# Performance work log

Hardware: AMD Instinct MI355X
Metric: run time of the kernel (lower is better)

## Reference

```python
import math
import jax, jax.numpy as jnp
import numpy as np

B, N, D, H, NUM_N, NUM_J = 16, 1024, 128, 8, 8, 4
PRE_S = 2.0


def setup_inputs() -> dict:
    key = jax.random.key(0)
    ks = jax.random.split(key, 12)
    g = lambda i, shape: jax.random.normal(ks[i], shape, jnp.float32) * 0.02
    return {
        "eigenvector": jax.random.normal(ks[0], (B, N, N), jnp.float32),
        "eigenvalue": jax.random.uniform(ks[1], (B, N), jnp.float32, minval=0.0, maxval=2.0),
        "length": jax.random.randint(ks[2], (B,), N // 2, N).at[0].set(N),
        "eig_w_W": g(3, (D, D + 1)), "eig_w_b": jnp.zeros((D,), jnp.float32),
        "ln1_s": jnp.ones((D,), jnp.float32), "ln1_b": jnp.zeros((D,), jnp.float32),
        "ln2_s": jnp.ones((D,), jnp.float32), "ln2_b": jnp.zeros((D,), jnp.float32),
        "qkv_W": g(4, (3 * D, D)), "qkv_b": jnp.zeros((3 * D,), jnp.float32),
        "out_W": g(5, (D, D)), "out_b": jnp.zeros((D,), jnp.float32),
        "ffn_W1": g(6, (D, D)), "ffn_b1": jnp.zeros((D,), jnp.float32),
        "ffn_W2": g(7, (D, D)), "ffn_b2": jnp.zeros((D,), jnp.float32),
        "dec_sca_W": g(8, (NUM_N, D)), "dec_sca_b": jnp.zeros((NUM_N,), jnp.float32),
        "dec_wav_W": g(9, (NUM_N, D)), "dec_wav_b": jnp.zeros((NUM_N,), jnp.float32),
        "dec_scl_W": g(10, (NUM_J, D)), "dec_scl_b": jnp.zeros((NUM_J,), jnp.float32),
    }


def _layernorm(x, s, b):
    m = x.mean(-1, keepdims=True)
    v = ((x - m) ** 2).mean(-1, keepdims=True)
    return (x - m) / jnp.sqrt(v + 1e-5) * s + b


def _gen_base(y, num_n):
    # Chebyshev-style recurrence; returns (base_wavelet, base_scaling), each [B, num_n, ...y.shape[1:]]
    t_even = jnp.ones_like(y)
    t_odd = y
    wav, sca = [t_even], [t_odd]
    for _ in range(num_n - 1):
        t_even = 2.0 * y * t_odd - t_even
        t_odd = 2.0 * y * t_even - t_odd
        wav.append(t_even)
        sca.append(t_odd)
    return jnp.stack(wav, 1), jnp.stack(sca, 1)


def _forward(eigenvalue, length,
             eig_w_W, eig_w_b, ln1_s, ln1_b, ln2_s, ln2_b,
             qkv_W, qkv_b, out_W, out_b, ffn_W1, ffn_b1, ffn_W2, ffn_b2,
             dec_sca_W, dec_sca_b, dec_wav_W, dec_wav_b, dec_scl_W, dec_scl_b):
    eva = eigenvalue  # [B, N], max(length) == N by construction
    pad = jnp.arange(N)[None, :] >= length[:, None]  # [B, N], True = padded key

    # --- SineEncoding ---
    div = jnp.exp(jnp.arange(0, D, 2).astype(jnp.float32) * (-math.log(10000.0) / D))  # [D/2]
    pe = (eva * 100.0)[:, :, None] * div  # [B, N, D/2]
    eeig = jnp.concatenate([eva[:, :, None], jnp.sin(pe), jnp.cos(pe)], -1)  # [B, N, D+1]
    eig = eeig @ eig_w_W.T + eig_w_b  # [B, N, D]

    # --- MHA block (pre-norm, key padding mask) ---
    h = _layernorm(eig, ln1_s, ln1_b)
    q, k, v = jnp.split(h @ qkv_W.T + qkv_b, 3, axis=-1)
    dh = D // H
    rh = lambda t: t.reshape(B, N, H, dh)
    scores = jnp.einsum('bqhd,bkhd->bhqk', rh(q), rh(k)) / math.sqrt(dh)
    scores = jnp.where(pad[:, None, None, :], -1e9, scores)  # finite mask (padded rows zeroed later)
    attn = jax.nn.softmax(scores, axis=-1)
    mo = jnp.einsum('bhqk,bkhd->bqhd', attn, rh(v)).reshape(B, N, D) @ out_W.T + out_b
    eig = eig + mo

    # --- FFN block ---
    f = _layernorm(eig, ln2_s, ln2_b)
    f = jax.nn.gelu(f @ ffn_W1.T + ffn_b1, approximate=False) @ ffn_W2.T + ffn_b2
    eig = eig + f

    lenf = length.astype(jnp.float32)[:, None]

    def pooled(W, b):
        c = eig @ W.T + b
        c = jnp.where(pad[:, :, None], 0.0, c)
        return c.sum(1) / (lenf + 1e-8)

    coe_sca = jax.nn.sigmoid(pooled(dec_sca_W, dec_sca_b))  # [B, NUM_N]
    coe_sca = coe_sca / (coe_sca.sum(-1, keepdims=True) + 1e-8)
    coe_wav = jax.nn.sigmoid(pooled(dec_wav_W, dec_wav_b))
    coe_wav = coe_wav / (coe_wav.sum(-1, keepdims=True) + 1e-8)
    coe_scl = jax.nn.sigmoid(pooled(dec_scl_W, dec_scl_b)) * PRE_S  # [B, NUM_J]

    _, base_scaling = _gen_base(eva[:, :, None] - 1.0, NUM_N)  # [B, NUM_N, N, 1]
    fsw = eva[:, :, None] * coe_scl[:, None, :]  # [B, N, NUM_J]
    fsw = jnp.where(fsw > 2.0, 0.0, fsw)
    base_wavelet, _ = _gen_base(fsw - 1.0, NUM_N)  # [B, NUM_N, N, NUM_J]

    base_scaling = 0.5 * (1.0 - base_scaling)
    base_wavelet = 0.5 * (1.0 - base_wavelet)
    curr_s = jnp.einsum('bn,bnxj->bxj', coe_sca, base_scaling)  # [B, N, 1]
    curr_w = jnp.einsum('bn,bnxj->bxj', coe_wav, base_wavelet)  # [B, N, NUM_J]
    out = jnp.concatenate([curr_s, curr_w], -1)  # [B, N, 1+NUM_J]
    out = out / (jnp.linalg.norm(out, axis=-1, keepdims=True) + 1e-8)  # tight_frames
    return out


def reference(eigenvector, eigenvalue, length,
              eig_w_W, eig_w_b, ln1_s, ln1_b, ln2_s, ln2_b,
              qkv_W, qkv_b, out_W, out_b, ffn_W1, ffn_b1, ffn_W2, ffn_b2,
              dec_sca_W, dec_sca_b, dec_wav_W, dec_wav_b, dec_scl_W, dec_scl_b):
    # eigenvector (evc_dense) is passed through unchanged in the original; the learned
    # output is filter_signals_after, which we return.
    return _forward(eigenvalue, length,
                    eig_w_W, eig_w_b, ln1_s, ln1_b, ln2_s, ln2_b,
                    qkv_W, qkv_b, out_W, out_b, ffn_W1, ffn_b1, ffn_W2, ffn_b2,
                    dec_sca_W, dec_sca_b, dec_wav_W, dec_wav_b, dec_scl_W, dec_scl_b)
```

## Files before the change

kernel.cpp:

```cpp
#include <hip/hip_runtime.h>
#include <math.h>

#define NB 16
#define NN 1024
#define ND 128
#define NH 8
#define DH 16

typedef float f32x4 __attribute__((ext_vector_type(4)));
typedef short s16x4 __attribute__((ext_vector_type(4)));

static __device__ __forceinline__ ushort f2bf(float x) {
  unsigned u = __float_as_uint(x);
  u = (u + 0x7FFFu + ((u >> 16) & 1u)) >> 16;
  return (ushort)u;
}

static __device__ __forceinline__ float exp2h(float x) {
  return __builtin_amdgcn_exp2f(x);
}

static __device__ __forceinline__ f32x4 mfma16(s16x4 a, s16x4 b, f32x4 c) {
  return __builtin_amdgcn_mfma_f32_16x16x16bf16_1k(a, b, c, 0, 0, 0);
}

static __device__ __forceinline__ s16x4 pack_bf4(float p0, float p1, float p2,
                                                 float p3) {
  s16x4 r = {(short)f2bf(p0), (short)f2bf(p1), (short)f2bf(p2),
             (short)f2bf(p3)};
  return r;
}

#define QSCALE 0.36067376022224085f

__global__ __launch_bounds__(256) void kW(
    const float* __restrict__ eW, const float* __restrict__ qkvW,
    const float* __restrict__ outW, const float* __restrict__ W1,
    const float* __restrict__ W2, ushort* __restrict__ wbf) {
  int i = blockIdx.x * 256 + threadIdx.x;
  if (i < 18432) {
    int r = i / 144, k = i - r * 144;
    wbf[i] = (k < 129) ? f2bf(eW[r * 129 + k]) : (ushort)0;
  } else if (i < 67584) {
    wbf[i] = f2bf(qkvW[i - 18432]);
  } else if (i < 83968) {
    wbf[i] = f2bf(outW[i - 67584]);
  } else if (i < 100352) {
    wbf[i] = f2bf(W1[i - 83968]);
  } else if (i < 116736) {
    wbf[i] = f2bf(W2[i - 100352]);
  }
}

__global__ __launch_bounds__(256, 4) void kA(
    const float* __restrict__ eva, const ushort* __restrict__ eWbf,
    const float* __restrict__ eb, const float* __restrict__ g1s,
    const float* __restrict__ g1b, const ushort* __restrict__ qkvbf,
    const float* __restrict__ qb, float* __restrict__ eig,
    ushort* __restrict__ qg, ushort* __restrict__ kg,
    ushort* __restrict__ vt) {
  __shared__ __align__(16) ushort ee[32][148];
  __shared__ __align__(16) float eig_f[32][132];
  __shared__ __align__(16) ushort hbf[32][132];
  int t = threadIdx.x;
  int rows0 = blockIdx.x * 32;
  int w = t >> 6, l = t & 63, g = l >> 4, c = l & 15;

  {
    int d = t & 63, r0 = t >> 6;
    float div = __expf((float)(2 * d) * (-9.210340371976184f / 128.0f));
#pragma unroll
    for (int k = 0; k < 8; ++k) {
      int row = r0 + 4 * k;
      float e = eva[rows0 + row];
      float pe = e * 100.0f * div;
      ee[row][1 + d] = f2bf(__sinf(pe));
      ee[row][65 + d] = f2bf(__cosf(pe));
      if (d == 0) ee[row][0] = f2bf(e);
    }
  }
  for (int i = t; i < 32 * 19; i += 256) {
    int row = i / 19, cc = 129 + (i - row * 19);
    ee[row][cc] = 0;
  }
  __syncthreads();

  {
    int rt = w >> 1;
#pragma unroll
    for (int i = 0; i < 4; ++i) {
      int ct = (w & 1) * 4 + i;
      f32x4 st = {0.f, 0.f, 0.f, 0.f};
#pragma unroll
      for (int kk = 0; kk < 9; ++kk) {
        s16x4 xf = *(const s16x4*)&ee[rt * 16 + c][kk * 16 + g * 4];
        s16x4 yf = *(const s16x4*)&eWbf[(ct * 16 + c) * 144 + kk * 16 + g * 4];
        st = mfma16(xf, yf, st);
      }
      float bias = eb[ct * 16 + c];
#pragma unroll
      for (int j = 0; j < 4; ++j)
        eig_f[rt * 16 + g * 4 + j][ct * 16 + c] = st[j] + bias;
    }
  }
  __syncthreads();

#pragma unroll
  for (int p = 0; p < 4; ++p) {
    int idx = p * 256 + t;
    int row = idx >> 5, c4 = idx & 31;
    *(float4*)&eig[(size_t)(rows0 + row) * ND + c4 * 4] =
        *(const float4*)&eig_f[row][c4 * 4];
  }

  {
    int row = t >> 3, s = t & 7;
    float vals[16];
    float sum = 0.f;
#pragma unroll
    for (int k = 0; k < 16; ++k) {
      vals[k] = eig_f[row][s + 8 * k];
      sum += vals[k];
    }
    sum += __shfl_xor(sum, 1, 8);
    sum += __shfl_xor(sum, 2, 8);
    sum += __shfl_xor(sum, 4, 8);
    float mean = sum * (1.0f / 128.0f);
    float sq = 0.f;
#pragma unroll
    for (int k = 0; k < 16; ++k) {
      float d = vals[k] - mean;
      sq += d * d;
    }
    sq += __shfl_xor(sq, 1, 8);
    sq += __shfl_xor(sq, 2, 8);
    sq += __shfl_xor(sq, 4, 8);
    float rstd = rsqrtf(sq * (1.0f / 128.0f) + 1e-5f);
#pragma unroll
    for (int k = 0; k < 16; ++k) {
      int col = s + 8 * k;
      hbf[row][col] = f2bf((vals[k] - mean) * rstd * g1s[col] + g1b[col]);
    }
  }
  __syncthreads();

  {
    int rt = w >> 1;
    int b = rows0 >> 10, nn0 = rows0 & 1023;
#pragma unroll
    for (int i = 0; i < 12; ++i) {
      int ct = (w & 1) * 12 + i;
      f32x4 st = {0.f, 0.f, 0.f, 0.f};
#pragma unroll
      for (int kk = 0; kk < 8; ++kk) {
        s16x4 xf = *(const s16x4*)&hbf[rt * 16 + c][kk * 16 + g * 4];
        s16x4 yf = *(const s16x4*)&qkvbf[(ct * 16 + c) * 128 + kk * 16 + g * 4];
        st = mfma16(xf, yf, st);
      }
      float bias = qb[ct * 16 + c];
      int which = ct >> 3, head = ct & 7;
      if (which == 2) {
        unsigned lo = (unsigned)f2bf(st[0] + bias) |
                      ((unsigned)f2bf(st[1] + bias) << 16);
        unsigned hi = (unsigned)f2bf(st[2] + bias) |
                      ((unsigned)f2bf(st[3] + bias) << 16);
        uint2 pk;
        pk.x = lo;
        pk.y = hi;
        *(uint2*)(vt + ((size_t)(b * NH + head) * DH + c) * NN + nn0 +
                  rt * 16 + g * 4) = pk;
      } else {
        ushort* dst = which == 0 ? qg : kg;
        float sc = which == 0 ? QSCALE : 1.0f;
        size_t base =
            ((size_t)(b * NH + head) * NN + nn0 + rt * 16 + g * 4) * DH + c;
#pragma unroll
        for (int j = 0; j < 4; ++j)
          dst[base + j * DH] = f2bf((st[j] + bias) * sc);
      }
    }
  }
}

__global__ __launch_bounds__(512) void k_attn(
    const ushort* __restrict__ qg, const ushort* __restrict__ kg,
    const ushort* __restrict__ vt, const int* __restrict__ length,
    ushort* __restrict__ att) {
  __shared__ ushort Ksh[128][20];
  __shared__ ushort VTsh[16][136];
  int bid = blockIdx.x;
  int bh = bid >> 3, qc = bid & 7;
  int b = bh >> 3, h = bh & 7;
  int t = threadIdx.x;
  int w = t >> 6, l = t & 63, g = l >> 4, c = l & 15;
  int len = length[b];
  int qrow = qc * 128 + w * 16 + c;
  s16x4 qf = *(const s16x4*)(qg + ((size_t)bh * NN + qrow) * DH + g * 4);
  f32x4 oacc = {0.f, 0.f, 0.f, 0.f};
  float lsum = 0.f;
  int ksr = t >> 2, ksc = t & 3;
  int vr = t >> 5, vc = t & 31;
  const ushort* kbg = kg + (size_t)bh * NN * DH;
  const ushort* vbg = vt + (size_t)bh * DH * NN;
  for (int t0 = 0; t0 < len; t0 += 128) {
    *(uint2*)&Ksh[ksr][ksc * 4] =
        *(const uint2*)(kbg + (size_t)(t0 + ksr) * DH + ksc * 4);
    *(uint2*)&VTsh[vr][vc * 4] =
        *(const uint2*)(vbg + (size_t)vr * NN + t0 + vc * 4);
    __syncthreads();
    if (t0 + 128 <= len) {
#pragma unroll
      for (int kt = 0; kt < 8; ++kt) {
        s16x4 kf = *(const s16x4*)&Ksh[kt * 16 + c][g * 4];
        f32x4 st = {0.f, 0.f, 0.f, 0.f};
        st = mfma16(kf, qf, st);
        float p0 = exp2h(st[0]), p1 = exp2h(st[1]);
        float p2 = exp2h(st[2]), p3 = exp2h(st[3]);
        lsum += (p0 + p1) + (p2 + p3);
        s16x4 pf = pack_bf4(p0, p1, p2, p3);
        s16x4 vf = *(const s16x4*)&VTsh[c][kt * 16 + g * 4];
        oacc = mfma16(vf, pf, oacc);
      }
    } else {
      for (int kt = 0; kt < 8 && t0 + kt * 16 < len; ++kt) {
        s16x4 kf = *(const s16x4*)&Ksh[kt * 16 + c][g * 4];
        f32x4 st = {0.f, 0.f, 0.f, 0.f};
        st = mfma16(kf, qf, st);
        int kj = t0 + kt * 16 + g * 4;
        float p0 = (kj + 0 < len) ? exp2h(st[0]) : 0.f;
        float p1 = (kj + 1 < len) ? exp2h(st[1]) : 0.f;
        float p2 = (kj + 2 < len) ? exp2h(st[2]) : 0.f;
        float p3 = (kj + 3 < len) ? exp2h(st[3]) : 0.f;
        lsum += (p0 + p1) + (p2 + p3);
        s16x4 pf = pack_bf4(p0, p1, p2, p3);
        s16x4 vf = *(const s16x4*)&VTsh[c][kt * 16 + g * 4];
        oacc = mfma16(vf, pf, oacc);
      }
    }
    __syncthreads();
  }
  lsum += __shfl_xor(lsum, 16, 64);
  lsum += __shfl_xor(lsum, 32, 64);
  float inv = 1.0f / lsum;
  s16x4 ob = pack_bf4(oacc[0] * inv, oacc[1] * inv, oacc[2] * inv,
                      oacc[3] * inv);
  *(s16x4*)(att + ((size_t)b * NN + qrow) * ND + h * DH + g * 4) = ob;
}

__global__ __launch_bounds__(256, 4) void kB(
    const ushort* __restrict__ attg, const ushort* __restrict__ outbf,
    const float* __restrict__ ob, const float* __restrict__ g2s,
    const float* __restrict__ g2b, const ushort* __restrict__ w1bf,
    const float* __restrict__ fb1, const ushort* __restrict__ w2bf,
    const float* __restrict__ fb2, const float* __restrict__ eig,
    const int* __restrict__ length, float* __restrict__ bsum) {
  __shared__ __align__(16) ushort attb[32][136];
  __shared__ __align__(16) float eig_f[32][132];
  __shared__ __align__(16) ushort hbf[32][132];
  __shared__ float csum[2][128];
  int t = threadIdx.x;
  int rows0 = blockIdx.x * 32;
  int w = t >> 6, l = t & 63, g = l >> 4, c = l & 15;
  int rt = w >> 1;

#pragma unroll
  for (int p = 0; p < 2; ++p) {
    int idx = p * 256 + t;
    int row = idx >> 4, c8 = idx & 15;
    *(uint4*)&attb[row][c8 * 8] =
        *(const uint4*)&attg[(size_t)(rows0 + row) * ND + c8 * 8];
  }
#pragma unroll
  for (int p = 0; p < 4; ++p) {
    int idx = p * 256 + t;
    int row = idx >> 5, c4 = idx & 31;
    *(float4*)&eig_f[row][c4 * 4] =
        *(const float4*)&eig[(size_t)(rows0 + row) * ND + c4 * 4];
  }
  __syncthreads();

#pragma unroll
  for (int i = 0; i < 4; ++i) {
    int ct = (w & 1) * 4 + i;
    f32x4 st = {0.f, 0.f, 0.f, 0.f};
#pragma unroll
    for (int kk = 0; kk < 8; ++kk) {
      s16x4 xf = *(const s16x4*)&attb[rt * 16 + c][kk * 16 + g * 4];
      s16x4 yf = *(const s16x4*)&outbf[(ct * 16 + c) * 128 + kk * 16 + g * 4];
      st = mfma16(xf, yf, st);
    }
    float bias = ob[ct * 16 + c];
#pragma unroll
    for (int j = 0; j < 4; ++j) {
      int row = rt * 16 + g * 4 + j, col = ct * 16 + c;
      eig_f[row][col] = st[j] + bias + eig_f[row][col];
    }
  }
  __syncthreads();

  {
    int row = t >> 3, s = t & 7;
    float vals[16];
    float sum = 0.f;
#pragma unroll
    for (int k = 0; k < 16; ++k) {
      vals[k] = eig_f[row][s + 8 * k];
      sum += vals[k];
    }
    sum += __shfl_xor(sum, 1, 8);
    sum += __shfl_xor(sum, 2, 8);
    sum += __shfl_xor(sum, 4, 8);
    float mean = sum * (1.0f / 128.0f);
    float sq = 0.f;
#pragma unroll
    for (int k = 0; k < 16; ++k) {
      float d = vals[k] - mean;
      sq += d * d;
    }
    sq += __shfl_xor(sq, 1, 8);
    sq += __shfl_xor(sq, 2, 8);
    sq += __shfl_xor(sq, 4, 8);
    float rstd = rsqrtf(sq * (1.0f / 128.0f) + 1e-5f);
#pragma unroll
    for (int k = 0; k < 16; ++k) {
      int col = s + 8 * k;
      hbf[row][col] = f2bf((vals[k] - mean) * rstd * g2s[col] + g2b[col]);
    }
  }
  __syncthreads();

#pragma unroll
  for (int i = 0; i < 4; ++i) {
    int ct = (w & 1) * 4 + i;
    f32x4 st = {0.f, 0.f, 0.f, 0.f};
#pragma unroll
    for (int kk = 0; kk < 8; ++kk) {
      s16x4 xf = *(const s16x4*)&hbf[rt * 16 + c][kk * 16 + g * 4];
      s16x4 yf = *(const s16x4*)&w1bf[(ct * 16 + c) * 128 + kk * 16 + g * 4];
      st = mfma16(xf, yf, st);
    }
    float bias = fb1[ct * 16 + c];
#pragma unroll
    for (int j = 0; j < 4; ++j) {
      float gv = st[j] + bias;
      attb[rt * 16 + g * 4 + j][ct * 16 + c] =
          f2bf(0.5f * gv * (1.0f + erff(gv * 0.7071067811865475f)));
    }
  }
  __syncthreads();

#pragma unroll
  for (int i = 0; i < 4; ++i) {
    int ct = (w & 1) * 4 + i;
    f32x4 st = {0.f, 0.f, 0.f, 0.f};
#pragma unroll
    for (int kk = 0; kk < 8; ++kk) {
      s16x4 xf = *(const s16x4*)&attb[rt * 16 + c][kk * 16 + g * 4];
      s16x4 yf = *(const s16x4*)&w2bf[(ct * 16 + c) * 128 + kk * 16 + g * 4];
      st = mfma16(xf, yf, st);
    }
    float bias = fb2[ct * 16 + c];
#pragma unroll
    for (int j = 0; j < 4; ++j) {
      int row = rt * 16 + g * 4 + j, col = ct * 16 + c;
      eig_f[row][col] = st[j] + bias + eig_f[row][col];
    }
  }
  __syncthreads();

  {
    int b = rows0 >> 10, n0 = rows0 & 1023;
    int len = length[b];
    int col = t & 127, half = t >> 7;
    float s = 0.f;
#pragma unroll
    for (int r = 0; r < 16; ++r) {
      int row = half * 16 + r;
      if (n0 + row < len) s += eig_f[row][col];
    }
    csum[half][col] = s;
  }
  __syncthreads();
  if (t < 128) bsum[(size_t)blockIdx.x * 128 + t] = csum[0][t] + csum[1][t];
}

__global__ __launch_bounds__(128) void kE(
    const float* __restrict__ bsum, const int* __restrict__ length,
    const float* __restrict__ dsW, const float* __restrict__ dsB,
    const float* __restrict__ dwW, const float* __restrict__ dwB,
    const float* __restrict__ dlW, const float* __restrict__ dlB,
    float* __restrict__ coe) {
  int b = blockIdx.x, t = threadIdx.x;
  __shared__ float s[128];
  __shared__ float pg[20];
  __shared__ float nrm[2];
  float a = 0.f;
#pragma unroll
  for (int c = 0; c < 32; ++c) a += bsum[(size_t)(b * 32 + c) * 128 + t];
  s[t] = a;
  __syncthreads();
  if (t < 20) {
    const float* W = t < 8 ? dsW + t * 128
                           : (t < 16 ? dwW + (t - 8) * 128 : dlW + (t - 16) * 128);
    float bias = t < 8 ? dsB[t] : (t < 16 ? dwB[t - 8] : dlB[t - 16]);
    float d = 0.f;
    for (int j = 0; j < 128; ++j) d += s[j] * W[j];
    float lf = (float)length[b];
    float pooled = (d + lf * bias) / (lf + 1e-8f);
    pg[t] = 1.f / (1.f + expf(-pooled));
  }
  __syncthreads();
  if (t == 0) {
    float a1 = 0.f, a2 = 0.f;
    for (int i = 0; i < 8; ++i) a1 += pg[i];
    for (int i = 8; i < 16; ++i) a2 += pg[i];
    nrm[0] = a1 + 1e-8f;
    nrm[1] = a2 + 1e-8f;
  }
  __syncthreads();
  if (t < 8) coe[b * 20 + t] = pg[t] / nrm[0];
  else if (t < 16) coe[b * 20 + t] = pg[t] / nrm[1];
  else if (t < 20) coe[b * 20 + t] = pg[t] * 2.0f;
}

__global__ __launch_bounds__(256) void k_wave(const float* __restrict__ eva,
                                              const float* __restrict__ coe,
                                              float* __restrict__ out) {
  int bn = blockIdx.x * 256 + threadIdx.x;
  int b = bn >> 10;
  float e = eva[bn];
  const float* cb = coe + b * 20;
  float y = e - 1.0f;
  float te = 1.0f, to = y;
  float cs = cb[0] * 0.5f * (1.0f - to);
#pragma unroll
  for (int i = 1; i < 8; ++i) {
    te = 2.f * y * to - te;
    to = 2.f * y * te - to;
    cs += cb[i] * 0.5f * (1.0f - to);
  }
  float cw[4];
#pragma unroll
  for (int j = 0; j < 4; ++j) {
    float fs = e * cb[16 + j];
    fs = (fs > 2.0f) ? 0.0f : fs;
    float yw = fs - 1.0f;
    float te2 = 1.0f, to2 = yw;
    float acc = 0.0f;
#pragma unroll
    for (int i = 1; i < 8; ++i) {
      te2 = 2.f * yw * to2 - te2;
      to2 = 2.f * yw * te2 - to2;
      acc += cb[8 + i] * 0.5f * (1.0f - te2);
    }
    cw[j] = acc;
  }
  float nrm = cs * cs + cw[0] * cw[0] + cw[1] * cw[1] + cw[2] * cw[2] +
              cw[3] * cw[3];
  float inv = 1.0f / (sqrtf(nrm) + 1e-8f);
  float* o = out + bn * 5;
  o[0] = cs * inv;
  o[1] = cw[0] * inv;
  o[2] = cw[1] * inv;
  o[3] = cw[2] * inv;
  o[4] = cw[3] * inv;
}

extern "C" void kernel_launch(void* const* d_in, const int* in_sizes, int n_in,
                              void* d_out, int out_size, void* d_ws,
                              size_t ws_size, hipStream_t stream) {
  const float* eva = (const float*)d_in[1];
  const int* length = (const int*)d_in[2];
  const float* eig_w_W = (const float*)d_in[3];
  const float* eig_w_b = (const float*)d_in[4];
  const float* ln1_s = (const float*)d_in[5];
  const float* ln1_b = (const float*)d_in[6];
  const float* ln2_s = (const float*)d_in[7];
  const float* ln2_b = (const float*)d_in[8];
  const float* qkv_W = (const float*)d_in[9];
  const float* qkv_b = (const float*)d_in[10];
  const float* out_W = (const float*)d_in[11];
  const float* out_b = (const float*)d_in[12];
  const float* ffn_W1 = (const float*)d_in[13];
  const float* ffn_b1 = (const float*)d_in[14];
  const float* ffn_W2 = (const float*)d_in[15];
  const float* ffn_b2 = (const float*)d_in[16];
  const float* dec_sca_W = (const float*)d_in[17];
  const float* dec_sca_b = (const float*)d_in[18];
  const float* dec_wav_W = (const float*)d_in[19];
  const float* dec_wav_b = (const float*)d_in[20];
  const float* dec_scl_W = (const float*)d_in[21];
  const float* dec_scl_b = (const float*)d_in[22];

  float* ws = (float*)d_ws;
  const size_t SZ = (size_t)NB * NN * ND;
  float* eig = ws;
  ushort* qg = (ushort*)(ws + SZ);
  ushort* kg = qg + SZ;
  ushort* vt = kg + SZ;
  ushort* attg = vt + SZ;
  float* bsum = (float*)(attg + SZ);
  float* coe = bsum + 512 * 128;
  ushort* wbf = (ushort*)(coe + 512);
  ushort* eWbf = wbf;
  ushort* qkvbf = wbf + 18432;
  ushort* outbf = wbf + 67584;
  ushort* w1bf = wbf + 83968;
  ushort* w2bf = wbf + 100352;

  kW<<<(116736 + 255) / 256, 256, 0, stream>>>(eig_w_W, qkv_W, out_W, ffn_W1,
                                               ffn_W2, wbf);
  kA<<<NB * NN / 32, 256, 0, stream>>>(eva, eWbf, eig_w_b, ln1_s, ln1_b, qkvbf,
                                       qkv_b, eig, qg, kg, vt);
  k_attn<<<NB * NH * 8, 512, 0, stream>>>(qg, kg, vt, length, attg);
  kB<<<NB * NN / 32, 256, 0, stream>>>(attg, outbf, out_b, ln2_s, ln2_b, w1bf,
                                       ffn_b1, w2bf, ffn_b2, eig, length, bsum);
  kE<<<NB, 128, 0, stream>>>(bsum, length, dec_sca_W, dec_sca_b, dec_wav_W,
                             dec_wav_b, dec_scl_W, dec_scl_b, coe);
  k_wave<<<(NB * NN) / 256, 256, 0, stream>>>(eva, coe, (float*)d_out);
}
```

Measured before the change: 99.61 us.

## Double-buffer K/V tiles in attention kernel and split MFMA accumulators

The attention kernel now keeps two LDS buffers for K and V^T. The next tile's global loads go into registers while MFMAs run on the current tile, and one barrier per iteration replaces two. The PV accumulation alternates between two accumulators to shorten the MFMA dependency chain, and s_setprio raises wave priority during the compute loop. The cost is more LDS and registers per block, which may reduce occupancy.

```diff
diff --git a/kernel.cpp b/kernel.cpp
--- a/kernel.cpp
+++ b/kernel.cpp
@@ -186,44 +186,62 @@
     const ushort* __restrict__ qg, const ushort* __restrict__ kg,
     const ushort* __restrict__ vt, const int* __restrict__ length,
     ushort* __restrict__ att) {
-  __shared__ ushort Ksh[128][20];
-  __shared__ ushort VTsh[16][136];
+  __shared__ ushort Ksh[2][128][20];
+  __shared__ ushort VTsh[2][16][136];
   int bid = blockIdx.x;
   int bh = bid >> 3, qc = bid & 7;
   int b = bh >> 3, h = bh & 7;
   int t = threadIdx.x;
   int w = t >> 6, l = t & 63, g = l >> 4, c = l & 15;
   int len = length[b];
+  int nt = (len + 127) >> 7;
   int qrow = qc * 128 + w * 16 + c;
   s16x4 qf = *(const s16x4*)(qg + ((size_t)bh * NN + qrow) * DH + g * 4);
-  f32x4 oacc = {0.f, 0.f, 0.f, 0.f};
+  f32x4 oacc0 = {0.f, 0.f, 0.f, 0.f};
+  f32x4 oacc1 = {0.f, 0.f, 0.f, 0.f};
   float lsum = 0.f;
   int ksr = t >> 2, ksc = t & 3;
   int vr = t >> 5, vc = t & 31;
   const ushort* kbg = kg + (size_t)bh * NN * DH;
   const ushort* vbg = vt + (size_t)bh * DH * NN;
-  for (int t0 = 0; t0 < len; t0 += 128) {
-    *(uint2*)&Ksh[ksr][ksc * 4] =
-        *(const uint2*)(kbg + (size_t)(t0 + ksr) * DH + ksc * 4);
-    *(uint2*)&VTsh[vr][vc * 4] =
-        *(const uint2*)(vbg + (size_t)vr * NN + t0 + vc * 4);
-    __syncthreads();
+
+  {
+    uint2 kv = *(const uint2*)(kbg + (size_t)ksr * DH + ksc * 4);
+    uint2 vv = *(const uint2*)(vbg + (size_t)vr * NN + vc * 4);
+    *(uint2*)&Ksh[0][ksr][ksc * 4] = kv;
+    *(uint2*)&VTsh[0][vr][vc * 4] = vv;
+  }
+  __syncthreads();
+
+  int cur = 0;
+  for (int ti = 0; ti < nt; ++ti) {
+    int t0 = ti << 7;
+    bool pre = (ti + 1 < nt);
+    uint2 kvn = {0u, 0u}, vvn = {0u, 0u};
+    if (pre) {
+      int t1 = t0 + 128;
+      kvn = *(const uint2*)(kbg + (size_t)(t1 + ksr) * DH + ksc * 4);
+      vvn = *(const uint2*)(vbg + (size_t)vr * NN + t1 + vc * 4);
+    }
     if (t0 + 128 <= len) {
+      __builtin_amdgcn_s_setprio(1);
 #pragma unroll
       for (int kt = 0; kt < 8; ++kt) {
-        s16x4 kf = *(const s16x4*)&Ksh[kt * 16 + c][g * 4];
+        s16x4 kf = *(const s16x4*)&Ksh[cur][kt * 16 + c][g * 4];
         f32x4 st = {0.f, 0.f, 0.f, 0.f};
         st = mfma16(kf, qf, st);
         float p0 = exp2h(st[0]), p1 = exp2h(st[1]);
         float p2 = exp2h(st[2]), p3 = exp2h(st[3]);
         lsum += (p0 + p1) + (p2 + p3);
         s16x4 pf = pack_bf4(p0, p1, p2, p3);
-        s16x4 vf = *(const s16x4*)&VTsh[c][kt * 16 + g * 4];
-        oacc = mfma16(vf, pf, oacc);
+        s16x4 vf = *(const s16x4*)&VTsh[cur][c][kt * 16 + g * 4];
+        if (kt & 1) oacc1 = mfma16(vf, pf, oacc1);
+        else oacc0 = mfma16(vf, pf, oacc0);
       }
+      __builtin_amdgcn_s_setprio(0);
     } else {
       for (int kt = 0; kt < 8 && t0 + kt * 16 < len; ++kt) {
-        s16x4 kf = *(const s16x4*)&Ksh[kt * 16 + c][g * 4];
+        s16x4 kf = *(const s16x4*)&Ksh[cur][kt * 16 + c][g * 4];
         f32x4 st = {0.f, 0.f, 0.f, 0.f};
         st = mfma16(kf, qf, st);
         int kj = t0 + kt * 16 + g * 4;
@@ -233,12 +251,20 @@
         float p3 = (kj + 3 < len) ? exp2h(st[3]) : 0.f;
         lsum += (p0 + p1) + (p2 + p3);
         s16x4 pf = pack_bf4(p0, p1, p2, p3);
-        s16x4 vf = *(const s16x4*)&VTsh[c][kt * 16 + g * 4];
-        oacc = mfma16(vf, pf, oacc);
+        s16x4 vf = *(const s16x4*)&VTsh[cur][c][kt * 16 + g * 4];
+        if (kt & 1) oacc1 = mfma16(vf, pf, oacc1);
+        else oacc0 = mfma16(vf, pf, oacc0);
       }
     }
-    __syncthreads();
-  }
+    if (pre) {
+      *(uint2*)&Ksh[cur ^ 1][ksr][ksc * 4] = kvn;
+      *(uint2*)&VTsh[cur ^ 1][vr][vc * 4] = vvn;
+      __syncthreads();
+      cur ^= 1;
+    }
+  }
+  f32x4 oacc = {oacc0[0] + oacc1[0], oacc0[1] + oacc1[1],
+                oacc0[2] + oacc1[2], oacc0[3] + oacc1[3]};
   lsum += __shfl_xor(lsum, 16, 64);
   lsum += __shfl_xor(lsum, 32, 64);
   float inv = 1.0f / lsum;
```

Result: no change. 100.2 us (+0.6%).
